# Performance work log

Measured on AMD Instinct MI355X. Metric: run time of the kernel, lower is better.

## Reference

```python
import jax, jax.numpy as jnp
import numpy as np

N_NODES = 50000
N_EDGES = 800000
D_IN = 256
D_HID = 256
D_OUT = 8


def _glorot(key, shape):
    fan_in = shape[-1]
    bound = 1.0 / np.sqrt(fan_in)
    return jax.random.uniform(key, shape, minval=-bound, maxval=bound, dtype=jnp.float32)


def setup_inputs() -> dict:
    key = jax.random.key(0)
    ks = jax.random.split(key, 12)
    x = jax.random.normal(ks[0], (N_NODES, D_IN), dtype=jnp.float32)
    edge_index = jax.random.randint(ks[1], (2, N_EDGES), 0, N_NODES, dtype=jnp.int64)
    return {
        "x": x,
        "edge_index": edge_index,
        # SAGEConv1: lin_l (neighbor path, has bias), lin_r (root path, no bias)
        "W1l": _glorot(ks[2], (D_HID, D_IN)),
        "b1": jnp.zeros((D_HID,), jnp.float32),
        "W1r": _glorot(ks[3], (D_HID, D_IN)),
        # SAGEConv2
        "W2l": _glorot(ks[4], (D_HID, D_HID)),
        "b2": jnp.zeros((D_HID,), jnp.float32),
        "W2r": _glorot(ks[5], (D_HID, D_HID)),
        # MLP decoder
        "Wm1": _glorot(ks[6], (D_HID, D_HID)),
        "bm1": _glorot(ks[7], (D_HID,)),
        "Wm2": _glorot(ks[8], (D_OUT, D_HID)),
        "bm2": _glorot(ks[9], (D_OUT,)),
    }


def _sage_conv(x, edge_index, Wl, b, Wr):
    # PyG SAGEConv with mean aggregation:
    # out = lin_l(mean_{j in N(i)} x_j) + lin_r(x_i)
    src, dst = edge_index[0], edge_index[1]
    msg = x[src]  # [E, d] gather
    agg = jax.ops.segment_sum(msg, dst, num_segments=x.shape[0])  # [N, d]
    cnt = jax.ops.segment_sum(jnp.ones((edge_index.shape[1],), x.dtype), dst,
                              num_segments=x.shape[0])  # in-degree [N]
    mean = agg / jnp.maximum(cnt, 1.0)[:, None]
    return mean @ Wl.T + b + x @ Wr.T


def reference(x, edge_index, W1l, b1, W1r, W2l, b2, W2r, Wm1, bm1, Wm2, bm2):
    h = jax.nn.relu(_sage_conv(x, edge_index, W1l, b1, W1r))
    h = jax.nn.relu(_sage_conv(h, edge_index, W2l, b2, W2r))
    h = jax.nn.relu(h @ Wm1.T + bm1)
    logits = h @ Wm2.T + bm2
    return jax.nn.softmax(logits, axis=-1)
```

## Files before the change

kernel.cpp:

```cpp
#include <hip/hip_runtime.h>
#include <hip/hip_bf16.h>
#include <cstdint>
#include <cstddef>

#define D 256

typedef __attribute__((ext_vector_type(8))) short bf16x8;
typedef __attribute__((ext_vector_type(4))) float f32x4;
typedef __attribute__((ext_vector_type(4))) unsigned short ushort4v;
typedef __attribute__((ext_vector_type(8))) unsigned short ushort8v;

__device__ __forceinline__ unsigned short f2bf(float f) {
  union { float f; unsigned int u; } v; v.f = f;
  unsigned int u = v.u;
  u += ((u >> 16) & 1u) + 0x7fffu;
  return (unsigned short)(u >> 16);
}
__device__ __forceinline__ float bf2f(unsigned short s) {
  union { unsigned int u; float f; } v; v.u = ((unsigned int)s) << 16;
  return v.f;
}

#define GLL16(g, l) __builtin_amdgcn_global_load_lds( \
    (const __attribute__((address_space(1))) void*)(g), \
    (__attribute__((address_space(3))) void*)(l), 16, 0, 0)


__global__ __launch_bounds__(256) void k_deg(const int* __restrict__ dst,
                                             int* __restrict__ deg, int E) {
  int e = blockIdx.x * 256 + threadIdx.x;
  if (e < E) atomicAdd(&deg[dst[e]], 1);
}

__global__ __launch_bounds__(256) void k_bsum(const int* __restrict__ deg,
                                              int* __restrict__ bsum, int M) {
  __shared__ int sm[256];
  int tid = threadIdx.x;
  int base = blockIdx.x * 1024 + tid * 4;
  int s = 0;
#pragma unroll
  for (int i = 0; i < 4; ++i) s += (base + i < M) ? deg[base + i] : 0;
  sm[tid] = s;
  __syncthreads();
  for (int off = 128; off > 0; off >>= 1) {
    if (tid < off) sm[tid] += sm[tid + off];
    __syncthreads();
  }
  if (tid == 0) bsum[blockIdx.x] = sm[0];
}

__global__ __launch_bounds__(64) void k_scanb(const int* __restrict__ bsum,
                                              int* __restrict__ boff,
                                              int* __restrict__ row_ptr,
                                              int nb, int M) {
  int l = threadIdx.x;
  int orig = (l < nb) ? bsum[l] : 0;
  int v = orig;
  for (int off = 1; off < 64; off <<= 1) {
    int t = __shfl_up(v, off);
    if (l >= off) v += t;
  }
  if (l < nb) boff[l] = v - orig;
  if (l == nb - 1) row_ptr[M] = v;
}

__global__ __launch_bounds__(256) void k_apply(const int* __restrict__ deg,
                                               const int* __restrict__ boff,
                                               int* __restrict__ row_ptr,
                                               int* __restrict__ cursor, int M) {
  __shared__ int sm[256];
  int tid = threadIdx.x;
  int base = blockIdx.x * 1024 + tid * 4;
  int d[4], p[4];
#pragma unroll
  for (int i = 0; i < 4; ++i) d[i] = (base + i < M) ? deg[base + i] : 0;
  p[0] = 0; p[1] = d[0]; p[2] = d[0] + d[1]; p[3] = d[0] + d[1] + d[2];
  int s = p[3] + d[3];
  sm[tid] = s;
  __syncthreads();
  for (int off = 1; off < 256; off <<= 1) {
    int t = (tid >= off) ? sm[tid - off] : 0;
    __syncthreads();
    sm[tid] += t;
    __syncthreads();
  }
  int excl = sm[tid] - s + boff[blockIdx.x];
#pragma unroll
  for (int i = 0; i < 4; ++i) {
    if (base + i < M) {
      row_ptr[base + i] = excl + p[i];
      cursor[base + i] = excl + p[i];
    }
  }
}

__global__ __launch_bounds__(256) void k_fill(const int* __restrict__ src,
                                              const int* __restrict__ dst,
                                              int* __restrict__ cursor,
                                              int* __restrict__ col, int E) {
  int e = blockIdx.x * 256 + threadIdx.x;
  if (e < E) {
    int p = atomicAdd(&cursor[dst[e]], 1);
    col[p] = src[e];
  }
}


__global__ __launch_bounds__(256) void k_split(const float* __restrict__ in,
                                               unsigned short* __restrict__ oh,
                                               unsigned short* __restrict__ ol,
                                               int n4) {
  int i = blockIdx.x * 256 + threadIdx.x;
  if (i >= n4) return;
  float4 v = ((const float4*)in)[i];
  float a[4] = {v.x, v.y, v.z, v.w};
  ushort4v h, l;
#pragma unroll
  for (int j = 0; j < 4; ++j) {
    h[j] = f2bf(a[j]);
    l[j] = f2bf(a[j] - bf2f(h[j]));
  }
  ((ushort4v*)oh)[i] = h;
  ((ushort4v*)ol)[i] = l;
}

__global__ __launch_bounds__(256) void k_splitw(
    const float* __restrict__ s0, const float* __restrict__ s1,
    const float* __restrict__ s2, const float* __restrict__ s3,
    const float* __restrict__ s4,
    unsigned short* __restrict__ h0, unsigned short* __restrict__ l0,
    unsigned short* __restrict__ h1, unsigned short* __restrict__ l1,
    unsigned short* __restrict__ h2, unsigned short* __restrict__ l2,
    unsigned short* __restrict__ h3, unsigned short* __restrict__ l3,
    unsigned short* __restrict__ h4, unsigned short* __restrict__ l4) {
  const float* s; unsigned short* oh; unsigned short* ol;
  switch (blockIdx.y) {
    case 0: s = s0; oh = h0; ol = l0; break;
    case 1: s = s1; oh = h1; ol = l1; break;
    case 2: s = s2; oh = h2; ol = l2; break;
    case 3: s = s3; oh = h3; ol = l3; break;
    default: s = s4; oh = h4; ol = l4; break;
  }
  int i = blockIdx.x * 256 + threadIdx.x;
  float4 v = ((const float4*)s)[i];
  float a[4] = {v.x, v.y, v.z, v.w};
  ushort4v h, l;
#pragma unroll
  for (int j = 0; j < 4; ++j) {
    h[j] = f2bf(a[j]);
    l[j] = f2bf(a[j] - bf2f(h[j]));
  }
  ((ushort4v*)oh)[i] = h;
  ((ushort4v*)ol)[i] = l;
}


__global__ __launch_bounds__(256) void k_gemm_mfma(
    const unsigned short* __restrict__ Ah, const unsigned short* __restrict__ Al,
    const unsigned short* __restrict__ Wh, const unsigned short* __restrict__ Wl,
    unsigned short* __restrict__ outBF, float* __restrict__ outF32,
    const float* __restrict__ bias, int M, int NBF, int NF, int relu,
    int nbxshift) {
  __shared__ char lds[32768];
  char* tA_h = lds;
  char* tA_l = lds + 8192;
  char* tW_h = lds + 16384;
  char* tW_l = lds + 24576;

  const int tid = threadIdx.x;
  const int wave = tid >> 6;
  const int lane = tid & 63;

  int nwg = gridDim.x;
  int id = blockIdx.x;
  int q = nwg >> 3, r = nwg & 7;
  int xcd = id & 7, j = id >> 3;
  int w = ((xcd < r) ? xcd * (q + 1) : r * (q + 1) + (xcd - r) * q) + j;
  const int by = w >> nbxshift;
  const int bx = w & ((1 << nbxshift) - 1);
  const int n0 = bx * 128;

  int aoff[2], woff[2], ldso[2];
#pragma unroll
  for (int rr = 0; rr < 2; ++rr) {
    int o = rr * 4096 + wave * 1024 + lane * 16;
    int row = o >> 6;
    int sp = (o >> 4) & 3;
    int sl = sp ^ ((row >> 1) & 3);
    int arow = by * 128 + row; if (arow > M - 1) arow = M - 1;
    aoff[rr] = arow * 256 + sl * 8;
    woff[rr] = (n0 + row) * 256 + sl * 8;
    ldso[rr] = rr * 4096 + wave * 1024;
  }

  const int rbase = (wave >> 1) * 64;
  const int cbase = (wave & 1) * 64;
  const int fr = lane & 15;
  const int g = lane >> 4;

  int a_addr[4], w_addr[4];
#pragma unroll
  for (int m = 0; m < 4; ++m) {
    int row = rbase + m * 16 + fr;
    a_addr[m] = row * 64 + ((g ^ ((row >> 1) & 3)) * 16);
  }
#pragma unroll
  for (int n = 0; n < 4; ++n) {
    int row = cbase + n * 16 + fr;
    w_addr[n] = row * 64 + ((g ^ ((row >> 1) & 3)) * 16);
  }

  f32x4 acc[4][4] = {};

#pragma unroll
  for (int rr = 0; rr < 2; ++rr) {
    GLL16(Ah + aoff[rr], tA_h + ldso[rr]);
    GLL16(Al + aoff[rr], tA_l + ldso[rr]);
    GLL16(Wh + woff[rr], tW_h + ldso[rr]);
    GLL16(Wl + woff[rr], tW_l + ldso[rr]);
  }

  for (int k0 = 0; k0 < 256; k0 += 32) {
    __syncthreads();
    bf16x8 ah[4], al[4], wh[4], wl[4];
#pragma unroll
    for (int m = 0; m < 4; ++m) {
      ah[m] = *(const bf16x8*)(tA_h + a_addr[m]);
      al[m] = *(const bf16x8*)(tA_l + a_addr[m]);
    }
#pragma unroll
    for (int n = 0; n < 4; ++n) {
      wh[n] = *(const bf16x8*)(tW_h + w_addr[n]);
      wl[n] = *(const bf16x8*)(tW_l + w_addr[n]);
    }
    __syncthreads();
    if (k0 < 224) {
      int ko = k0 + 32;
#pragma unroll
      for (int rr = 0; rr < 2; ++rr) {
        GLL16(Ah + aoff[rr] + ko, tA_h + ldso[rr]);
        GLL16(Al + aoff[rr] + ko, tA_l + ldso[rr]);
        GLL16(Wh + woff[rr] + ko, tW_h + ldso[rr]);
        GLL16(Wl + woff[rr] + ko, tW_l + ldso[rr]);
      }
    }
#pragma unroll
    for (int m = 0; m < 4; ++m)
#pragma unroll
      for (int n = 0; n < 4; ++n) {
        acc[m][n] = __builtin_amdgcn_mfma_f32_16x16x32_bf16(ah[m], wh[n], acc[m][n], 0, 0, 0);
        acc[m][n] = __builtin_amdgcn_mfma_f32_16x16x32_bf16(ah[m], wl[n], acc[m][n], 0, 0, 0);
        acc[m][n] = __builtin_amdgcn_mfma_f32_16x16x32_bf16(al[m], wh[n], acc[m][n], 0, 0, 0);
      }
  }

#pragma unroll
  for (int n = 0; n < 4; ++n) {
    int col = n0 + cbase + n * 16 + fr;
    bool isbf = col < NBF;
    int fcol = col - NBF;
    float bv = (!isbf && bias) ? bias[fcol] : 0.f;
#pragma unroll
    for (int m = 0; m < 4; ++m) {
      f32x4 a = acc[m][n];
#pragma unroll
      for (int rr = 0; rr < 4; ++rr) {
        int row = by * 128 + rbase + m * 16 + g * 4 + rr;
        if (row < M) {
          if (isbf) {
            outBF[(size_t)row * NBF + col] = f2bf(a[rr]);
          } else {
            float v = a[rr] + bv;
            if (relu) v = fmaxf(v, 0.f);
            outF32[(size_t)row * NF + fcol] = v;
          }
        }
      }
    }
  }
}


__global__ __launch_bounds__(256) void k_agg2(const unsigned short* __restrict__ T1,
                                              const float* __restrict__ T2,
                                              unsigned short* __restrict__ Hh,
                                              unsigned short* __restrict__ Hl,
                                              const int* __restrict__ row_ptr,
                                              const int* __restrict__ col, int M) {
  int wave = threadIdx.x >> 6, lane = threadIdx.x & 63;
  int n = blockIdx.x * 4 + wave;
  if (n >= M) return;
  int beg = row_ptr[n], end = row_ptr[n + 1];
  int half = lane >> 5, sl = lane & 31;
  float s[8] = {0.f, 0.f, 0.f, 0.f, 0.f, 0.f, 0.f, 0.f};
  for (int j = beg + half; j < end; j += 2) {
    int srcr = col[j];
    ushort8v v = *(const ushort8v*)(T1 + (size_t)srcr * 256 + sl * 8);
#pragma unroll
    for (int i = 0; i < 8; ++i) s[i] += bf2f(v[i]);
  }
#pragma unroll
  for (int i = 0; i < 8; ++i) s[i] += __shfl_xor(s[i], 32);
  int dg = end - beg;
  float inv = 1.0f / (float)(dg > 0 ? dg : 1);
  const float4* t2p = (const float4*)(T2 + (size_t)n * 256 + sl * 8);
  float4 ta = t2p[0], tb = t2p[1];
  float h[8];
  h[0] = fmaxf(s[0] * inv + ta.x, 0.f);
  h[1] = fmaxf(s[1] * inv + ta.y, 0.f);
  h[2] = fmaxf(s[2] * inv + ta.z, 0.f);
  h[3] = fmaxf(s[3] * inv + ta.w, 0.f);
  h[4] = fmaxf(s[4] * inv + tb.x, 0.f);
  h[5] = fmaxf(s[5] * inv + tb.y, 0.f);
  h[6] = fmaxf(s[6] * inv + tb.z, 0.f);
  h[7] = fmaxf(s[7] * inv + tb.w, 0.f);
  if (half == 0) {
    ushort8v hh;
#pragma unroll
    for (int i = 0; i < 8; ++i) hh[i] = f2bf(h[i]);
    *(ushort8v*)(Hh + (size_t)n * 256 + sl * 8) = hh;
  } else {
    ushort8v hl;
#pragma unroll
    for (int i = 0; i < 8; ++i) {
      unsigned short hi = f2bf(h[i]);
      hl[i] = f2bf(h[i] - bf2f(hi));
    }
    *(ushort8v*)(Hl + (size_t)n * 256 + sl * 8) = hl;
  }
}


__global__ __launch_bounds__(256) void k_final(const float* __restrict__ H,
                                               const float* __restrict__ Wm2,
                                               const float* __restrict__ bm2,
                                               float* __restrict__ out, int M) {
  int node = blockIdx.x * 4 + (threadIdx.x >> 6);
  int lane = threadIdx.x & 63;
  if (node >= M) return;
  int o = lane >> 3;
  int r = lane & 7;
  const float* h = H + (size_t)node * D;
  const float* w = Wm2 + (size_t)o * D;
  float p = 0.f;
  for (int k = r; k < D; k += 8) p += h[k] * w[k];
  p += __shfl_xor(p, 1);
  p += __shfl_xor(p, 2);
  p += __shfl_xor(p, 4);
  float logit = p + bm2[o];
  float m = logit;
  m = fmaxf(m, __shfl_xor(m, 8));
  m = fmaxf(m, __shfl_xor(m, 16));
  m = fmaxf(m, __shfl_xor(m, 32));
  float e = expf(logit - m);
  float s = e;
  s += __shfl_xor(s, 8);
  s += __shfl_xor(s, 16);
  s += __shfl_xor(s, 32);
  if (r == 0) out[(size_t)node * 8 + o] = e / s;
}


extern "C" void kernel_launch(void* const* d_in, const int* in_sizes, int n_in,
                              void* d_out, int out_size, void* d_ws, size_t ws_size,
                              hipStream_t stream) {
  const float* x   = (const float*)d_in[0];
  const int*   ei  = (const int*)d_in[1];
  const float* W1l = (const float*)d_in[2];
  const float* b1  = (const float*)d_in[3];
  const float* W1r = (const float*)d_in[4];
  const float* W2l = (const float*)d_in[5];
  const float* b2  = (const float*)d_in[6];
  const float* W2r = (const float*)d_in[7];
  const float* Wm1 = (const float*)d_in[8];
  const float* bm1 = (const float*)d_in[9];
  const float* Wm2 = (const float*)d_in[10];
  const float* bm2 = (const float*)d_in[11];
  float* out = (float*)d_out;

  int M = in_sizes[0] / D;
  int E = in_sizes[1] / 2;
  const int* src = ei;
  const int* dst = ei + E;

  char* p = (char*)d_ws;
  auto alloc = [&](size_t bytes) {
    char* q = p;
    p += (bytes + 255) & ~(size_t)255;
    return q;
  };
  unsigned short* bh0  = (unsigned short*)alloc((size_t)M * 256 * 2);
  unsigned short* bh1  = (unsigned short*)alloc((size_t)M * 256 * 2);
  unsigned short* T1bf = (unsigned short*)alloc((size_t)M * 256 * 2);
  float*          T2f  = (float*)alloc((size_t)M * 256 * 4);
  unsigned short* Wc1h = (unsigned short*)alloc(512 * 256 * 2);
  unsigned short* Wc1l = (unsigned short*)alloc(512 * 256 * 2);
  unsigned short* Wc2h = (unsigned short*)alloc(512 * 256 * 2);
  unsigned short* Wc2l = (unsigned short*)alloc(512 * 256 * 2);
  unsigned short* Wm1h = (unsigned short*)alloc(256 * 256 * 2);
  unsigned short* Wm1l = (unsigned short*)alloc(256 * 256 * 2);
  int* deg     = (int*)alloc((size_t)M * 4);
  int* row_ptr = (int*)alloc((size_t)(M + 1) * 4);
  int* cursor  = (int*)alloc((size_t)M * 4);
  int* col     = (int*)alloc((size_t)E * 4);
  int* bsum    = (int*)alloc(64 * 4);
  int* boff    = (int*)alloc(64 * 4);

  int nb = (M + 1023) / 1024;

  hipMemsetAsync(deg, 0, (size_t)M * sizeof(int), stream);
  k_deg<<<dim3((E + 255) / 256), dim3(256), 0, stream>>>(dst, deg, E);
  k_bsum<<<dim3(nb), dim3(256), 0, stream>>>(deg, bsum, M);
  k_scanb<<<dim3(1), dim3(64), 0, stream>>>(bsum, boff, row_ptr, nb, M);
  k_apply<<<dim3(nb), dim3(256), 0, stream>>>(deg, boff, row_ptr, cursor, M);
  k_fill<<<dim3((E + 255) / 256), dim3(256), 0, stream>>>(src, dst, cursor, col, E);

  int nx4 = M * 256 / 4;
  k_split<<<dim3((nx4 + 255) / 256), dim3(256), 0, stream>>>(x, bh0, bh1, nx4);
  k_splitw<<<dim3(64, 5), dim3(256), 0, stream>>>(
      W1l, W1r, W2l, W2r, Wm1,
      Wc1h, Wc1l, Wc1h + 65536, Wc1l + 65536,
      Wc2h, Wc2l, Wc2h + 65536, Wc2l + 65536,
      Wm1h, Wm1l);

  dim3 blk(256);
  int nwg4 = ((M + 127) / 128) * 4;
  int nwg2 = ((M + 127) / 128) * 2;
  int aggGrid = (M + 3) / 4;

  k_gemm_mfma<<<dim3(nwg4), blk, 0, stream>>>(bh0, bh1, Wc1h, Wc1l, T1bf, T2f, b1, M, 256, 256, 0, 2);
  k_agg2<<<dim3(aggGrid), blk, 0, stream>>>(T1bf, T2f, bh0, bh1, row_ptr, col, M);
  k_gemm_mfma<<<dim3(nwg4), blk, 0, stream>>>(bh0, bh1, Wc2h, Wc2l, T1bf, T2f, b2, M, 256, 256, 0, 2);
  k_agg2<<<dim3(aggGrid), blk, 0, stream>>>(T1bf, T2f, bh0, bh1, row_ptr, col, M);
  k_gemm_mfma<<<dim3(nwg2), blk, 0, stream>>>(bh0, bh1, Wm1h, Wm1l, nullptr, T2f, bm1, M, 0, 256, 1, 1);
  k_final<<<dim3((M + 3) / 4), blk, 0, stream>>>(T2f, Wm2, bm2, out, M);
}
```

Baseline: 580.4 us.

## Double-buffer GEMM LDS tiles and unroll neighbor gather in aggregation

The MFMA GEMM now uses two 32 KB LDS buffers so the next K-slice is loaded with global_load_lds while the current slice is consumed. Explicit vmcnt waits and raw barriers replace the two __syncthreads per iteration, so global latency can overlap compute. The aggregation kernel unrolls its edge loop by two to keep two independent gathers in flight per half-wave. The cost is doubled LDS per block (64 KB), which may reduce occupancy, plus manual wait counts that must match the number of outstanding loads.

```diff
diff --git a/kernel.cpp b/kernel.cpp
--- a/kernel.cpp
+++ b/kernel.cpp
@@ -161,11 +161,7 @@
     unsigned short* __restrict__ outBF, float* __restrict__ outF32,
     const float* __restrict__ bias, int M, int NBF, int NF, int relu,
     int nbxshift) {
-  __shared__ char lds[32768];
-  char* tA_h = lds;
-  char* tA_l = lds + 8192;
-  char* tW_h = lds + 16384;
-  char* tW_l = lds + 24576;
+  __shared__ char lds[65536];
 
   const int tid = threadIdx.x;
   const int wave = tid >> 6;
@@ -214,35 +210,40 @@
 
 #pragma unroll
   for (int rr = 0; rr < 2; ++rr) {
-    GLL16(Ah + aoff[rr], tA_h + ldso[rr]);
-    GLL16(Al + aoff[rr], tA_l + ldso[rr]);
-    GLL16(Wh + woff[rr], tW_h + ldso[rr]);
-    GLL16(Wl + woff[rr], tW_l + ldso[rr]);
-  }
-
-  for (int k0 = 0; k0 < 256; k0 += 32) {
-    __syncthreads();
+    GLL16(Ah + aoff[rr], lds + 0     + ldso[rr]);
+    GLL16(Al + aoff[rr], lds + 8192  + ldso[rr]);
+    GLL16(Wh + woff[rr], lds + 16384 + ldso[rr]);
+    GLL16(Wl + woff[rr], lds + 24576 + ldso[rr]);
+  }
+
+  for (int t = 0; t < 8; ++t) {
+    const int cb = (t & 1) * 32768;
+    if (t < 7) {
+      const int nb = ((t + 1) & 1) * 32768;
+      const int ko = (t + 1) * 32;
+#pragma unroll
+      for (int rr = 0; rr < 2; ++rr) {
+        GLL16(Ah + aoff[rr] + ko, lds + nb + 0     + ldso[rr]);
+        GLL16(Al + aoff[rr] + ko, lds + nb + 8192  + ldso[rr]);
+        GLL16(Wh + woff[rr] + ko, lds + nb + 16384 + ldso[rr]);
+        GLL16(Wl + woff[rr] + ko, lds + nb + 24576 + ldso[rr]);
+      }
+      asm volatile("s_waitcnt vmcnt(8)" ::: "memory");
+    } else {
+      asm volatile("s_waitcnt vmcnt(0)" ::: "memory");
+    }
+    __builtin_amdgcn_s_barrier();
+
     bf16x8 ah[4], al[4], wh[4], wl[4];
 #pragma unroll
     for (int m = 0; m < 4; ++m) {
-      ah[m] = *(const bf16x8*)(tA_h + a_addr[m]);
-      al[m] = *(const bf16x8*)(tA_l + a_addr[m]);
+      ah[m] = *(const bf16x8*)(lds + cb + 0    + a_addr[m]);
+      al[m] = *(const bf16x8*)(lds + cb + 8192 + a_addr[m]);
     }
 #pragma unroll
     for (int n = 0; n < 4; ++n) {
-      wh[n] = *(const bf16x8*)(tW_h + w_addr[n]);
-      wl[n] = *(const bf16x8*)(tW_l + w_addr[n]);
-    }
-    __syncthreads();
-    if (k0 < 224) {
-      int ko = k0 + 32;
-#pragma unroll
-      for (int rr = 0; rr < 2; ++rr) {
-        GLL16(Ah + aoff[rr] + ko, tA_h + ldso[rr]);
-        GLL16(Al + aoff[rr] + ko, tA_l + ldso[rr]);
-        GLL16(Wh + woff[rr] + ko, tW_h + ldso[rr]);
-        GLL16(Wl + woff[rr] + ko, tW_l + ldso[rr]);
-      }
+      wh[n] = *(const bf16x8*)(lds + cb + 16384 + w_addr[n]);
+      wl[n] = *(const bf16x8*)(lds + cb + 24576 + w_addr[n]);
     }
 #pragma unroll
     for (int m = 0; m < 4; ++m)
@@ -252,6 +253,7 @@
         acc[m][n] = __builtin_amdgcn_mfma_f32_16x16x32_bf16(ah[m], wl[n], acc[m][n], 0, 0, 0);
         acc[m][n] = __builtin_amdgcn_mfma_f32_16x16x32_bf16(al[m], wh[n], acc[m][n], 0, 0, 0);
       }
+    __builtin_amdgcn_s_barrier();
   }
 
 #pragma unroll
@@ -293,11 +295,20 @@
   int beg = row_ptr[n], end = row_ptr[n + 1];
   int half = lane >> 5, sl = lane & 31;
   float s[8] = {0.f, 0.f, 0.f, 0.f, 0.f, 0.f, 0.f, 0.f};
-  for (int j = beg + half; j < end; j += 2) {
-    int srcr = col[j];
-    ushort8v v = *(const ushort8v*)(T1 + (size_t)srcr * 256 + sl * 8);
-#pragma unroll
-    for (int i = 0; i < 8; ++i) s[i] += bf2f(v[i]);
+  int j = beg + half;
+  for (; j + 2 < end; j += 4) {
+    int i0 = col[j];
+    int i1 = col[j + 2];
+    ushort8v v0 = *(const ushort8v*)(T1 + (size_t)i0 * 256 + sl * 8);
+    ushort8v v1 = *(const ushort8v*)(T1 + (size_t)i1 * 256 + sl * 8);
+#pragma unroll
+    for (int i = 0; i < 8; ++i) s[i] += bf2f(v0[i]) + bf2f(v1[i]);
+  }
+  for (; j < end; j += 2) {
+    int i0 = col[j];
+    ushort8v v0 = *(const ushort8v*)(T1 + (size_t)i0 * 256 + sl * 8);
+#pragma unroll
+    for (int i = 0; i < 8; ++i) s[i] += bf2f(v0[i]);
   }
 #pragma unroll
   for (int i = 0; i < 8; ++i) s[i] += __shfl_xor(s[i], 32);
```

After: 571.0 us. Within noise of the previous version (-1.6%).
